# Performance work log

Measured on AMD Instinct MI355X. Metric: run time of the kernel, lower is better.

The kernel has to match this reference:

```python
import jax, jax.numpy as jnp
import numpy as np

LPC_ORDER = 24  # M; k has last dim M+1


def setup_inputs() -> dict:
    key = jax.random.key(0)
    k = jax.random.normal(key, (2097152, LPC_ORDER + 1), dtype=jnp.float32)
    return {"k": k}


def reference(k) -> jnp.ndarray:
    # PARCOR -> LPC Levinson recursion.
    # a = k.clone(); for m in 2..M: a[1:m] += k[m] * flip(a[1:m])
    # Note: a[..., m] is never written before step m, so k[..., m] == a[..., m].
    M = k.shape[-1] - 1
    a = k
    for m in range(2, M + 1):  # small static loop over coefficient order
        am = a[..., 1:m]
        km = k[..., m:m + 1]
        a = a.at[..., 1:m].set(am + km * am[..., ::-1])
    return a
```

## Files before the change

kernel.cpp:

```cpp
#include <hip/hip_runtime.h>

#define ORDER 24
#define W 25
#define ROWS_PER_BLOCK 256
#define THREADS 256

__global__ __launch_bounds__(THREADS)
void parcor2lpc_kernel(const float* __restrict__ in,
                       float* __restrict__ out, int rows)
{
    __shared__ float lds[ROWS_PER_BLOCK * W];

    const int t = threadIdx.x;
    const long long row0 = (long long)blockIdx.x * ROWS_PER_BLOCK;
    const long long base = row0 * W;
    const long long rem  = (long long)rows - row0;
    const int nrows = rem >= ROWS_PER_BLOCK ? ROWS_PER_BLOCK : (int)rem;

    if (nrows == ROWS_PER_BLOCK) {
        const float4* __restrict__ gin = (const float4*)(in + base);
        float4* sv = (float4*)lds;
        #pragma unroll
        for (int i = t; i < (ROWS_PER_BLOCK * W) / 4; i += THREADS)
            sv[i] = gin[i];
    } else {
        for (int i = t; i < nrows * W; i += THREADS)
            lds[i] = in[base + i];
    }
    __syncthreads();

    if (t < nrows) {
        float a[W];
        #pragma unroll
        for (int j = 0; j < W; ++j) a[j] = lds[t * W + j];

        #pragma unroll
        for (int m = 2; m <= ORDER; ++m) {
            const float km = a[m];
            #pragma unroll
            for (int j = 1; j <= (m - 1) / 2; ++j) {
                const float lo = a[j], hi = a[m - j];
                a[j]     = fmaf(km, hi, lo);
                a[m - j] = fmaf(km, lo, hi);
            }
            if ((m & 1) == 0) {
                const float v = a[m / 2];
                a[m / 2] = fmaf(km, v, v);
            }
        }

        #pragma unroll
        for (int j = 0; j < W; ++j) lds[t * W + j] = a[j];
    }
    __syncthreads();

    if (nrows == ROWS_PER_BLOCK) {
        float4* __restrict__ gout = (float4*)(out + base);
        const float4* sv = (const float4*)lds;
        #pragma unroll
        for (int i = t; i < (ROWS_PER_BLOCK * W) / 4; i += THREADS)
            gout[i] = sv[i];
    } else {
        for (int i = t; i < nrows * W; i += THREADS)
            out[base + i] = lds[i];
    }
}

extern "C" void kernel_launch(void* const* d_in, const int* in_sizes, int n_in,
                              void* d_out, int out_size, void* d_ws, size_t ws_size,
                              hipStream_t stream) {
    const float* k = (const float*)d_in[0];
    float* out = (float*)d_out;
    const int rows = in_sizes[0] / W;
    const int grid = (rows + ROWS_PER_BLOCK - 1) / ROWS_PER_BLOCK;
    parcor2lpc_kernel<<<grid, THREADS, 0, stream>>>(k, out, rows);
}
```

Measured before the change: 344.5 us.

## Use direct global-to-LDS loads and per-wave staging without block barriers

Full blocks now load input straight into LDS with the global_load_lds builtin. Each wave stages only its own 64 rows, so both block-wide __syncthreads are replaced by a per-wave vmcnt wait. Register round-trips for the copy and cross-wave barrier stalls go away, so waves proceed independently. The risk is subtle: correctness depends on per-wave LDS visibility after the vmcnt wait, with no LDS fence or wave barrier. The partial-block path keeps the old synchronized scheme.

```diff
diff --git a/kernel.cpp b/kernel.cpp
--- a/kernel.cpp
+++ b/kernel.cpp
@@ -4,63 +4,86 @@
 #define W 25
 #define ROWS_PER_BLOCK 256
 #define THREADS 256
+#define WAVE_FLOATS (64 * W)
+
+__device__ __forceinline__ void levinson(float* __restrict__ a)
+{
+    #pragma unroll
+    for (int m = 2; m <= ORDER; ++m) {
+        const float km = a[m];
+        #pragma unroll
+        for (int j = 1; j <= (m - 1) / 2; ++j) {
+            const float lo = a[j], hi = a[m - j];
+            a[j]     = fmaf(km, hi, lo);
+            a[m - j] = fmaf(km, lo, hi);
+        }
+        if ((m & 1) == 0) {
+            const float v = a[m / 2];
+            a[m / 2] = fmaf(km, v, v);
+        }
+    }
+}
 
 __global__ __launch_bounds__(THREADS)
 void parcor2lpc_kernel(const float* __restrict__ in,
                        float* __restrict__ out, int rows)
 {
-    __shared__ float lds[ROWS_PER_BLOCK * W];
+    __shared__ __align__(16) float lds[ROWS_PER_BLOCK * W];
 
-    const int t = threadIdx.x;
+    const int t    = threadIdx.x;
+    const int wave = t >> 6;
+    const int lane = t & 63;
     const long long row0 = (long long)blockIdx.x * ROWS_PER_BLOCK;
     const long long base = row0 * W;
     const long long rem  = (long long)rows - row0;
     const int nrows = rem >= ROWS_PER_BLOCK ? ROWS_PER_BLOCK : (int)rem;
 
     if (nrows == ROWS_PER_BLOCK) {
-        const float4* __restrict__ gin = (const float4*)(in + base);
-        float4* sv = (float4*)lds;
+        const int wbase = wave * WAVE_FLOATS;
+        const float* __restrict__ gw = in + base + wbase;
+
         #pragma unroll
-        for (int i = t; i < (ROWS_PER_BLOCK * W) / 4; i += THREADS)
-            sv[i] = gin[i];
-    } else {
-        for (int i = t; i < nrows * W; i += THREADS)
-            lds[i] = in[base + i];
-    }
-    __syncthreads();
+        for (int k = 0; k < 6; ++k) {
+            __builtin_amdgcn_global_load_lds(
+                (const __attribute__((address_space(1))) void*)(gw + k * 256 + lane * 4),
+                (__attribute__((address_space(3))) void*)(&lds[wbase + k * 256]),
+                16, 0, 0);
+        }
+        __builtin_amdgcn_global_load_lds(
+            (const __attribute__((address_space(1))) void*)(gw + 1536 + lane),
+            (__attribute__((address_space(3))) void*)(&lds[wbase + 1536]),
+            4, 0, 0);
 
-    if (t < nrows) {
+        asm volatile("s_waitcnt vmcnt(0)" ::: "memory");
+
         float a[W];
         #pragma unroll
         for (int j = 0; j < W; ++j) a[j] = lds[t * W + j];
 
-        #pragma unroll
-        for (int m = 2; m <= ORDER; ++m) {
-            const float km = a[m];
-            #pragma unroll
-            for (int j = 1; j <= (m - 1) / 2; ++j) {
-                const float lo = a[j], hi = a[m - j];
-                a[j]     = fmaf(km, hi, lo);
-                a[m - j] = fmaf(km, lo, hi);
-            }
-            if ((m & 1) == 0) {
-                const float v = a[m / 2];
-                a[m / 2] = fmaf(km, v, v);
-            }
-        }
+        levinson(a);
 
         #pragma unroll
         for (int j = 0; j < W; ++j) lds[t * W + j] = a[j];
-    }
-    __syncthreads();
 
-    if (nrows == ROWS_PER_BLOCK) {
         float4* __restrict__ gout = (float4*)(out + base);
         const float4* sv = (const float4*)lds;
+        const int f0 = wave * (WAVE_FLOATS / 4);
         #pragma unroll
-        for (int i = t; i < (ROWS_PER_BLOCK * W) / 4; i += THREADS)
-            gout[i] = sv[i];
+        for (int k = 0; k < 6; ++k)
+            gout[f0 + k * 64 + lane] = sv[f0 + k * 64 + lane];
+        if (lane < 16)
+            gout[f0 + 384 + lane] = sv[f0 + 384 + lane];
     } else {
+        for (int i = t; i < nrows * W; i += THREADS)
+            lds[i] = in[base + i];
+        __syncthreads();
+        if (t < nrows) {
+            float a[W];
+            for (int j = 0; j < W; ++j) a[j] = lds[t * W + j];
+            levinson(a);
+            for (int j = 0; j < W; ++j) lds[t * W + j] = a[j];
+        }
+        __syncthreads();
         for (int i = t; i < nrows * W; i += THREADS)
             out[base + i] = lds[i];
     }
```

New measurement: 341.2 us. Within noise of the previous version (-1.0%).
